# Kernel tuning notes

Hardware: AMD Instinct MI355X
Metric: run time of the kernel (lower is better)

The kernel has to match this reference:

```python
import jax, jax.numpy as jnp
import numpy as np

OUTCOMES = [8, 8, 8, 8, 8, 8]           # concept outcome counts (concepts_order)
N_TOTAL = int(np.prod(OUTCOMES))        # 262144 joint states
N_VALID = 8192                          # admissible states
B, D = 4096, 1024


def setup_inputs() -> dict:
    key = jax.random.key(0)
    k1, k2 = jax.random.split(key)
    embeddings = jax.random.normal(k1, (B, D), dtype=jnp.float32)
    W = jax.random.normal(k2, (N_VALID, D), dtype=jnp.float32) * 0.02
    b = jnp.zeros((N_VALID,), dtype=jnp.float32)
    # unique sorted admissible-state indices, like torch.argwhere(mask)
    rng = np.random.default_rng(0)
    valid_states = jnp.asarray(
        np.sort(rng.choice(N_TOTAL, size=N_VALID, replace=False)).astype(np.int32))
    return {"embeddings": embeddings, "W": W, "b": b, "valid_states": valid_states}


def reference(embeddings, W, b, valid_states):
    # softmax over valid states: [B, N_VALID]
    probs = jax.nn.softmax(embeddings @ W.T + b, axis=1)
    probs_t = probs.T  # [N_VALID, B] for leading-axis segment reduction
    marginals = []
    stride = N_TOTAL
    for n_i in OUTCOMES:
        stride //= n_i
        # digit of each valid joint-state index along this concept's axis
        digit = (valid_states // stride) % n_i  # [N_VALID]
        # equivalent to scattering probs into the full joint tensor and
        # summing over all other concept axes, without materializing it
        m = jax.ops.segment_sum(probs_t, digit, num_segments=n_i).T  # [B, n_i]
        marginals.append(m)
    return jnp.stack(marginals)  # [n_concepts, B, 8]
```

## Files before the change

### kernel.cpp

```cpp
#include <hip/hip_runtime.h>
#include <hip/hip_bf16.h>
#include <cstdint>
#include <cstddef>

typedef __bf16 bf16_t;
typedef bf16_t bf16x8 __attribute__((ext_vector_type(8)));
typedef bf16_t bf16x4 __attribute__((ext_vector_type(4)));
typedef float  f32x4  __attribute__((ext_vector_type(4)));
typedef unsigned int u32;

#define BROWS 4096
#define NV    8192
#define KD    1024
#define KSPLIT 16
#define NT    16

#define GLL(gsrc, ldst) \
  __builtin_amdgcn_global_load_lds((const __attribute__((address_space(1))) u32*)(gsrc), \
                                   (__attribute__((address_space(3))) u32*)(ldst), 16, 0, 0)

__global__ void cvt_kernel(const float* __restrict__ src, bf16_t* __restrict__ dst, int n4) {
  int idx = blockIdx.x * blockDim.x + threadIdx.x;
  int stride = gridDim.x * blockDim.x;
  for (int i = idx; i < n4; i += stride) {
    float4 v = ((const float4*)src)[i];
    bf16x4 o;
    o[0] = (bf16_t)v.x; o[1] = (bf16_t)v.y; o[2] = (bf16_t)v.z; o[3] = (bf16_t)v.w;
    ((bf16x4*)dst)[i] = o;
  }
}

__global__ void build_st_kernel(const int* __restrict__ vstate, bf16_t* __restrict__ st) {
  int g = blockIdx.x * blockDim.x + threadIdx.x;
  if (g >= 48 * NV) return;
  int bucket = g >> 13;
  int j = g & (NV - 1);
  int c = bucket >> 3;
  int d = bucket & 7;
  int dig = (vstate[j] >> (15 - 3 * c)) & 7;
  st[g] = (bf16_t)(dig == d ? 1.0f : 0.0f);
}

__global__ __launch_bounds__(512, 2)
void gemm_exp_kernel(const bf16_t* __restrict__ A, const bf16_t* __restrict__ B,
                     const float* __restrict__ bias, bf16_t* __restrict__ expout) {
  __shared__ __align__(16) char lds[2][65536];

  const int t    = threadIdx.x;
  const int lane = t & 63;
  const int wv   = t >> 6;
  const int wm   = wv >> 2;
  const int wn   = wv & 3;
  const int fr   = lane & 15;
  const int fq   = lane >> 4;

  int bid = blockIdx.x;
  int wg  = (bid & 7) * 64 + (bid >> 3);
  const int mt = wg >> 5;
  const int nt = wg & 31;
  const int row0 = mt * 256;
  const int col0 = nt * 256;

  const int c    = lane ^ ((lane >> 3) & 7);
  const int srow = c >> 3;
  const int skel = (c & 7) * 8;
  const bf16_t* gsrc0 = (wv < 4)
      ? A + (size_t)(row0 + wv * 64 + srow) * KD + skel
      : B + (size_t)(col0 + (wv - 4) * 64 + srow) * KD + skel;

  const int frs = (fr & 7) << 4;
  int aoff[2], boff[2];
#pragma unroll
  for (int kh = 0; kh < 2; ++kh) {
    const int sw = (fr * 128 + kh * 64 + fq * 16) ^ frs;
    aoff[kh] = wm * 16384 + sw;
    boff[kh] = 32768 + wn * 8192 + sw;
  }

  f32x4 acc[8][4] = {};

  {
#pragma unroll
    for (int j = 0; j < 8; ++j)
      GLL(gsrc0 + (size_t)j * 8 * KD, &lds[0][wv * 8192 + j * 1024]);
  }
  asm volatile("s_waitcnt vmcnt(0)" ::: "memory");
  __builtin_amdgcn_s_barrier();
  asm volatile("" ::: "memory");

  int cur = 0;
  for (int kt = 0; kt < NT; ++kt) {
    if (kt + 1 < NT) {
#pragma unroll
      for (int j = 0; j < 8; ++j)
        GLL(gsrc0 + (size_t)j * 8 * KD + (kt + 1) * 64, &lds[cur ^ 1][wv * 8192 + j * 1024]);
      asm volatile("s_waitcnt vmcnt(8)" ::: "memory");
    } else {
      asm volatile("s_waitcnt vmcnt(0)" ::: "memory");
    }
    __builtin_amdgcn_s_barrier();
    asm volatile("" ::: "memory");

    const char* bufp = &lds[cur][0];
    bf16x8 bfrag[2][4];
#pragma unroll
    for (int kh = 0; kh < 2; ++kh)
#pragma unroll
      for (int n = 0; n < 4; ++n)
        bfrag[kh][n] = *(const bf16x8*)(bufp + boff[kh] + n * 2048);

#pragma unroll
    for (int mg = 0; mg < 8; mg += 2) {
      bf16x8 af[2][2];
#pragma unroll
      for (int kh = 0; kh < 2; ++kh)
#pragma unroll
        for (int mi = 0; mi < 2; ++mi)
          af[kh][mi] = *(const bf16x8*)(bufp + aoff[kh] + (mg + mi) * 2048);
      __builtin_amdgcn_s_setprio(1);
#pragma unroll
      for (int mi = 0; mi < 2; ++mi)
#pragma unroll
        for (int n = 0; n < 4; ++n)
#pragma unroll
          for (int kh = 0; kh < 2; ++kh)
            acc[mg + mi][n] = __builtin_amdgcn_mfma_f32_16x16x32_bf16(
                af[kh][mi], bfrag[kh][n], acc[mg + mi][n], 0, 0, 0);
      __builtin_amdgcn_s_setprio(0);
    }

    asm volatile("" ::: "memory");
    __builtin_amdgcn_s_barrier();
    asm volatile("" ::: "memory");
    cur ^= 1;
  }

#pragma unroll
  for (int n = 0; n < 4; ++n) {
    const int col = col0 + wn * 64 + n * 16 + fr;
    const float bb = bias[col];
#pragma unroll
    for (int m = 0; m < 8; ++m) {
      const int rowb = row0 + wm * 128 + m * 16 + fq * 4;
#pragma unroll
      for (int r = 0; r < 4; ++r) {
        float e = exp2f((acc[m][n][r] + bb) * 1.44269504088896340736f);
        expout[(size_t)(rowb + r) * NV + col] = (bf16_t)e;
      }
    }
  }
}

__global__ __launch_bounds__(256)
void marginal_mfma_kernel(const bf16_t* __restrict__ expbuf, const bf16_t* __restrict__ st,
                          float* __restrict__ part) {
  __shared__ bf16_t sE[128][32];
  __shared__ bf16_t sS[48][32];

  const int t    = threadIdx.x;
  const int lane = t & 63;
  const int wv   = t >> 6;

  const int rt = blockIdx.x >> 4;
  const int ks = blockIdx.x & (KSPLIT - 1);
  const int row0 = rt * 128;
  const int kbase = ks * (NV / KSPLIT);

  const int srow = t >> 2;
  const int skel = (t & 3) * 8;
  const bf16_t* ep0 = expbuf + (size_t)(row0 + srow) * NV + kbase + skel;
  const bf16_t* ep1 = ep0 + (size_t)64 * NV;
  const bf16_t* sp0 = st + (size_t)srow * NV + kbase + skel;
  bf16_t* se0 = &sE[0][0] + (wv * 64) * 8;
  bf16_t* se1 = &sE[0][0] + (256 + wv * 64) * 8;
  bf16_t* ss0 = &sS[0][0] + (wv * 64) * 8;

  const int fr = lane & 15;
  const int fq = lane >> 4;

  f32x4 acc[2][3] = {};

  for (int kk = 0; kk < NV / KSPLIT; kk += 32) {
    GLL(ep0 + kk, se0);
    GLL(ep1 + kk, se1);
    if (wv < 3) GLL(sp0 + kk, ss0);
    __syncthreads();

    bf16x8 af[2], bg[3];
#pragma unroll
    for (int m = 0; m < 2; ++m)
      af[m] = *(const bf16x8*)&sE[wv * 32 + m * 16 + fr][fq * 8];
#pragma unroll
    for (int n = 0; n < 3; ++n)
      bg[n] = *(const bf16x8*)&sS[n * 16 + fr][fq * 8];
#pragma unroll
    for (int m = 0; m < 2; ++m)
#pragma unroll
      for (int n = 0; n < 3; ++n)
        acc[m][n] = __builtin_amdgcn_mfma_f32_16x16x32_bf16(af[m], bg[n], acc[m][n], 0, 0, 0);
    __syncthreads();
  }

  float* pbase = part + (size_t)ks * BROWS * 48;
#pragma unroll
  for (int m = 0; m < 2; ++m) {
    const int rowb = row0 + wv * 32 + m * 16 + fq * 4;
#pragma unroll
    for (int n = 0; n < 3; ++n) {
      const int bucket = n * 16 + fr;
#pragma unroll
      for (int r = 0; r < 4; ++r)
        pbase[(size_t)(rowb + r) * 48 + bucket] = acc[m][n][r];
    }
  }
}

__global__ __launch_bounds__(64)
void reduce_kernel(const float* __restrict__ part, float* __restrict__ out) {
  const int b = blockIdx.x;
  const int t = threadIdx.x;
  __shared__ float fin[48];
  if (t < 48) {
    float s = 0.f;
#pragma unroll
    for (int ks = 0; ks < KSPLIT; ++ks)
      s += part[((size_t)ks * BROWS + b) * 48 + t];
    fin[t] = s;
  }
  __syncthreads();
  if (t < 48) {
    float total = fin[0] + fin[1] + fin[2] + fin[3] + fin[4] + fin[5] + fin[6] + fin[7];
    out[(size_t)(t >> 3) * BROWS * 8 + (size_t)b * 8 + (t & 7)] = fin[t] / total;
  }
}

extern "C" void kernel_launch(void* const* d_in, const int* in_sizes, int n_in,
                              void* d_out, int out_size, void* d_ws, size_t ws_size,
                              hipStream_t stream) {
  const float* E    = (const float*)d_in[0];
  const float* W    = (const float*)d_in[1];
  const float* bias = (const float*)d_in[2];
  const int*   vs   = (const int*)d_in[3];
  float* out = (float*)d_out;

  char* ws = (char*)d_ws;
  size_t off = 0;
  bf16_t* Eb     = (bf16_t*)(ws + off); off += (size_t)BROWS * KD * 2;
  bf16_t* Wb     = (bf16_t*)(ws + off); off += (size_t)NV * KD * 2;
  bf16_t* expbuf = (bf16_t*)(ws + off); off += (size_t)BROWS * NV * 2;
  bf16_t* st     = (bf16_t*)(ws + off); off += (size_t)48 * NV * 2;
  float*  part   = (float*)(ws + off);  off += (size_t)KSPLIT * BROWS * 48 * 4;

  build_st_kernel<<<(48 * NV + 255) / 256, 256, 0, stream>>>(vs, st);
  cvt_kernel<<<2048, 256, 0, stream>>>(E, Eb, BROWS * KD / 4);
  cvt_kernel<<<2048, 256, 0, stream>>>(W, Wb, NV * KD / 4);
  gemm_exp_kernel<<<512, 512, 0, stream>>>(Eb, Wb, bias, expbuf);
  marginal_mfma_kernel<<<32 * KSPLIT, 256, 0, stream>>>(expbuf, st, part);
  reduce_kernel<<<BROWS, 64, 0, stream>>>(part, out);
}
```

Measured before the change: 123.7 us.

## Restructure GEMM main loop into four staged sub-phases with interleaved prefetch

The GEMM mainloop is split into four sub-phases per K-tile (A/B halves by K-half and M-half). Each phase issues part of the next tile's global-to-LDS loads, separated by barriers, so loads spread across the MFMA work instead of being issued in one burst. The LDS layout changes to K-half-major blocks with a new XOR swizzle, and fragments are loaded per phase to cut register pressure. The cost is many more barriers per iteration and finer-grained vmcnt waits, which could stall waves if the waits are miscounted.

```diff
diff --git a/kernel.cpp b/kernel.cpp
--- a/kernel.cpp
+++ b/kernel.cpp
@@ -18,6 +18,7 @@
 #define GLL(gsrc, ldst) \
   __builtin_amdgcn_global_load_lds((const __attribute__((address_space(1))) u32*)(gsrc), \
                                    (__attribute__((address_space(3))) u32*)(ldst), 16, 0, 0)
+#define FENCE asm volatile("" ::: "memory")
 
 __global__ void cvt_kernel(const float* __restrict__ src, bf16_t* __restrict__ dst, int n4) {
   int idx = blockIdx.x * blockDim.x + threadIdx.x;
@@ -45,6 +46,10 @@
 void gemm_exp_kernel(const bf16_t* __restrict__ A, const bf16_t* __restrict__ B,
                      const float* __restrict__ bias, bf16_t* __restrict__ expout) {
   __shared__ __align__(16) char lds[2][65536];
+  #define AKH0 0
+  #define AKH1 16384
+  #define BKH0 32768
+  #define BKH1 49152
 
   const int t    = threadIdx.x;
   const int lane = t & 63;
@@ -61,77 +66,117 @@
   const int row0 = mt * 256;
   const int col0 = nt * 256;
 
-  const int c    = lane ^ ((lane >> 3) & 7);
-  const int srow = c >> 3;
-  const int skel = (c & 7) * 8;
-  const bf16_t* gsrc0 = (wv < 4)
-      ? A + (size_t)(row0 + wv * 64 + srow) * KD + skel
-      : B + (size_t)(col0 + (wv - 4) * 64 + srow) * KD + skel;
-
-  const int frs = (fr & 7) << 4;
-  int aoff[2], boff[2];
-#pragma unroll
-  for (int kh = 0; kh < 2; ++kh) {
-    const int sw = (fr * 128 + kh * 64 + fq * 16) ^ frs;
-    aoff[kh] = wm * 16384 + sw;
-    boff[kh] = 32768 + wn * 8192 + sw;
-  }
+  const int srow = lane >> 2;
+  const int skel = ((lane & 3) ^ ((lane >> 3) & 3)) * 8;
+  const bf16_t* aptr = A + (size_t)(row0 + wv * 32 + srow) * KD + skel;
+  const bf16_t* bptr = B + (size_t)(col0 + wv * 32 + srow) * KD + skel;
+  const int dchunk = (wv * 2) * 1024;
+
+  const int xsw = (fr & 6) << 3;
+  const int base_a = (((wm * 128 + fr) * 64 + fq * 16) ^ xsw);
+  const int base_b = 32768 + (((wn * 64 + fr) * 64 + fq * 16) ^ xsw);
 
   f32x4 acc[8][4] = {};
 
-  {
-#pragma unroll
-    for (int j = 0; j < 8; ++j)
-      GLL(gsrc0 + (size_t)j * 8 * KD, &lds[0][wv * 8192 + j * 1024]);
-  }
-  asm volatile("s_waitcnt vmcnt(0)" ::: "memory");
+  GLL(aptr, &lds[0][AKH0 + dchunk]);
+  GLL(aptr + 16 * KD, &lds[0][AKH0 + dchunk + 1024]);
+  GLL(bptr, &lds[0][BKH0 + dchunk]);
+  GLL(bptr + 16 * KD, &lds[0][BKH0 + dchunk + 1024]);
+  GLL(aptr + 32, &lds[0][AKH1 + dchunk]);
+  GLL(aptr + 32 + 16 * KD, &lds[0][AKH1 + dchunk + 1024]);
+  GLL(bptr + 32, &lds[0][BKH1 + dchunk]);
+  GLL(bptr + 32 + 16 * KD, &lds[0][BKH1 + dchunk + 1024]);
+  asm volatile("s_waitcnt vmcnt(4)" ::: "memory");
   __builtin_amdgcn_s_barrier();
-  asm volatile("" ::: "memory");
+  FENCE;
 
   int cur = 0;
   for (int kt = 0; kt < NT; ++kt) {
-    if (kt + 1 < NT) {
-#pragma unroll
-      for (int j = 0; j < 8; ++j)
-        GLL(gsrc0 + (size_t)j * 8 * KD + (kt + 1) * 64, &lds[cur ^ 1][wv * 8192 + j * 1024]);
-      asm volatile("s_waitcnt vmcnt(8)" ::: "memory");
-    } else {
-      asm volatile("s_waitcnt vmcnt(0)" ::: "memory");
-    }
-    __builtin_amdgcn_s_barrier();
-    asm volatile("" ::: "memory");
-
-    const char* bufp = &lds[cur][0];
-    bf16x8 bfrag[2][4];
-#pragma unroll
-    for (int kh = 0; kh < 2; ++kh)
+    const char* bufp = lds[cur];
+    char* nbuf = lds[cur ^ 1];
+    const bf16_t* anext = aptr + (kt + 1) * 64;
+    const bf16_t* bnext = bptr + (kt + 1) * 64;
+    const bool pf = (kt + 1 < NT);
+
+    bf16x8 bfrag[4], af[4];
+
+#pragma unroll
+    for (int n = 0; n < 4; ++n)
+      bfrag[n] = *(const bf16x8*)(bufp + base_b + n * 1024);
+#pragma unroll
+    for (int mi = 0; mi < 4; ++mi)
+      af[mi] = *(const bf16x8*)(bufp + base_a + mi * 1024);
+    if (pf) {
+      GLL(anext, &nbuf[AKH0 + dchunk]);
+      GLL(anext + 16 * KD, &nbuf[AKH0 + dchunk + 1024]);
+    }
+    FENCE; __builtin_amdgcn_s_barrier(); FENCE;
+    __builtin_amdgcn_s_setprio(1);
+#pragma unroll
+    for (int mi = 0; mi < 4; ++mi)
 #pragma unroll
       for (int n = 0; n < 4; ++n)
-        bfrag[kh][n] = *(const bf16x8*)(bufp + boff[kh] + n * 2048);
-
-#pragma unroll
-    for (int mg = 0; mg < 8; mg += 2) {
-      bf16x8 af[2][2];
-#pragma unroll
-      for (int kh = 0; kh < 2; ++kh)
-#pragma unroll
-        for (int mi = 0; mi < 2; ++mi)
-          af[kh][mi] = *(const bf16x8*)(bufp + aoff[kh] + (mg + mi) * 2048);
-      __builtin_amdgcn_s_setprio(1);
-#pragma unroll
-      for (int mi = 0; mi < 2; ++mi)
-#pragma unroll
-        for (int n = 0; n < 4; ++n)
-#pragma unroll
-          for (int kh = 0; kh < 2; ++kh)
-            acc[mg + mi][n] = __builtin_amdgcn_mfma_f32_16x16x32_bf16(
-                af[kh][mi], bfrag[kh][n], acc[mg + mi][n], 0, 0, 0);
-      __builtin_amdgcn_s_setprio(0);
-    }
-
-    asm volatile("" ::: "memory");
-    __builtin_amdgcn_s_barrier();
-    asm volatile("" ::: "memory");
+        acc[mi][n] = __builtin_amdgcn_mfma_f32_16x16x32_bf16(af[mi], bfrag[n], acc[mi][n], 0, 0, 0);
+    __builtin_amdgcn_s_setprio(0);
+    FENCE; __builtin_amdgcn_s_barrier(); FENCE;
+
+#pragma unroll
+    for (int mi = 0; mi < 4; ++mi)
+      af[mi] = *(const bf16x8*)(bufp + base_a + (4 + mi) * 1024);
+    if (pf) {
+      GLL(bnext, &nbuf[BKH0 + dchunk]);
+      GLL(bnext + 16 * KD, &nbuf[BKH0 + dchunk + 1024]);
+    }
+    FENCE; __builtin_amdgcn_s_barrier(); FENCE;
+    __builtin_amdgcn_s_setprio(1);
+#pragma unroll
+    for (int mi = 0; mi < 4; ++mi)
+#pragma unroll
+      for (int n = 0; n < 4; ++n)
+        acc[4 + mi][n] = __builtin_amdgcn_mfma_f32_16x16x32_bf16(af[mi], bfrag[n], acc[4 + mi][n], 0, 0, 0);
+    __builtin_amdgcn_s_setprio(0);
+    if (pf) asm volatile("s_waitcnt vmcnt(4)" ::: "memory");
+    else    asm volatile("s_waitcnt vmcnt(0)" ::: "memory");
+    FENCE; __builtin_amdgcn_s_barrier(); FENCE;
+
+#pragma unroll
+    for (int n = 0; n < 4; ++n)
+      bfrag[n] = *(const bf16x8*)(bufp + base_b + 16384 + n * 1024);
+#pragma unroll
+    for (int mi = 0; mi < 4; ++mi)
+      af[mi] = *(const bf16x8*)(bufp + base_a + 16384 + mi * 1024);
+    if (pf) {
+      GLL(anext + 32, &nbuf[AKH1 + dchunk]);
+      GLL(anext + 32 + 16 * KD, &nbuf[AKH1 + dchunk + 1024]);
+    }
+    FENCE; __builtin_amdgcn_s_barrier(); FENCE;
+    __builtin_amdgcn_s_setprio(1);
+#pragma unroll
+    for (int mi = 0; mi < 4; ++mi)
+#pragma unroll
+      for (int n = 0; n < 4; ++n)
+        acc[mi][n] = __builtin_amdgcn_mfma_f32_16x16x32_bf16(af[mi], bfrag[n], acc[mi][n], 0, 0, 0);
+    __builtin_amdgcn_s_setprio(0);
+    FENCE; __builtin_amdgcn_s_barrier(); FENCE;
+
+#pragma unroll
+    for (int mi = 0; mi < 4; ++mi)
+      af[mi] = *(const bf16x8*)(bufp + base_a + 16384 + (4 + mi) * 1024);
+    if (pf) {
+      GLL(bnext + 32, &nbuf[BKH1 + dchunk]);
+      GLL(bnext + 32 + 16 * KD, &nbuf[BKH1 + dchunk + 1024]);
+    }
+    FENCE; __builtin_amdgcn_s_barrier(); FENCE;
+    __builtin_amdgcn_s_setprio(1);
+#pragma unroll
+    for (int mi = 0; mi < 4; ++mi)
+#pragma unroll
+      for (int n = 0; n < 4; ++n)
+        acc[4 + mi][n] = __builtin_amdgcn_mfma_f32_16x16x32_bf16(af[mi], bfrag[n], acc[4 + mi][n], 0, 0, 0);
+    __builtin_amdgcn_s_setprio(0);
+    if (pf) asm volatile("s_waitcnt vmcnt(4)" ::: "memory");
+    FENCE; __builtin_amdgcn_s_barrier(); FENCE;
+
     cur ^= 1;
   }
 
```

Result: no change. 122.4 us (-1.0%).
